# Kernel optimization log

Hardware: AMD Instinct MI355X
Metric: run time of the kernel (lower is better)

## Reference

```python
import jax, jax.numpy as jnp
import numpy as np

B, H, W, C = 1, 72, 72, 768
NH, HD = 12, 64
FF = 3072
EPS = 1e-6
THETA = 10000.0
S = H * W


def _rope_tables():
    freqs = 1.0 / THETA ** (np.arange(0, HD, 4, dtype=np.float32) / HD)  # [16]
    t = np.arange(H, dtype=np.float32)
    fx = np.outer(t, freqs)  # [72,16]
    fy = np.outer(t, freqs)
    fx = np.tile(fx[:, None, :], (1, W, 1))  # [72,72,16]
    fy = np.tile(fy[None, :, :], (H, 1, 1))
    fxy = np.concatenate([fx, fy], axis=-1).reshape(S, -1)  # [5184,32]
    fxy = np.repeat(fxy, 2, axis=-1)  # [5184,64]
    return jnp.asarray(np.cos(fxy)), jnp.asarray(np.sin(fxy))


def _rotate_pairwise(x):
    x1 = x[..., ::2]
    x2 = x[..., 1::2]
    return jnp.stack([-x2, x1], axis=-1).reshape(x.shape)


def _layernorm(x, g, b):
    m = jnp.mean(x, axis=-1, keepdims=True)
    v = jnp.mean(jnp.square(x - m), axis=-1, keepdims=True)
    return (x - m) * jax.lax.rsqrt(v + EPS) * g + b


def setup_inputs() -> dict:
    key = jax.random.key(0)
    ks = jax.random.split(key, 12)
    s_c = 1.0 / np.sqrt(C)
    s_ff = 1.0 / np.sqrt(FF)
    d = {
        "hidden_states": jax.random.normal(ks[0], (B, H, W, C), jnp.float32),
        "wq": jax.random.normal(ks[1], (C, C), jnp.float32) * s_c,
        "bq": jnp.zeros((C,), jnp.float32),
        "wk": jax.random.normal(ks[2], (C, C), jnp.float32) * s_c,
        "bk": jnp.zeros((C,), jnp.float32),
        "wv": jax.random.normal(ks[3], (C, C), jnp.float32) * s_c,
        "bv": jnp.zeros((C,), jnp.float32),
        "wo": jax.random.normal(ks[4], (C, C), jnp.float32) * s_c,
        "bo": jnp.zeros((C,), jnp.float32),
        "g1": jnp.ones((C,), jnp.float32),
        "b1": jnp.zeros((C,), jnp.float32),
        "g2": jnp.ones((C,), jnp.float32),
        "b2": jnp.zeros((C,), jnp.float32),
        "w_fc1": jax.random.normal(ks[5], (C, FF), jnp.float32) * s_c,
        "b_fc1": jnp.zeros((FF,), jnp.float32),
        "w_fc2": jax.random.normal(ks[6], (FF, C), jnp.float32) * s_ff,
        "b_fc2": jnp.zeros((C,), jnp.float32),
        "ls1": jnp.full((C,), 1e-5, jnp.float32),
        "ls2": jnp.full((C,), 1e-5, jnp.float32),
    }
    return d


def reference(hidden_states, wq, bq, wk, bk, wv, bv, wo, bo, g1, b1, g2, b2,
              w_fc1, b_fc1, w_fc2, b_fc2, ls1, ls2):
    cos, sin = _rope_tables()  # [S, HD]
    cos = cos[None, None]  # [1,1,S,HD]
    sin = sin[None, None]

    residual = hidden_states
    x = hidden_states.reshape(B, S, C)
    x = _layernorm(x, g1, b1)

    # attention
    q = (x @ wq + bq).reshape(B, S, NH, HD).transpose(0, 2, 1, 3)
    k = (x @ wk + bk).reshape(B, S, NH, HD).transpose(0, 2, 1, 3)
    v = (x @ wv + bv).reshape(B, S, NH, HD).transpose(0, 2, 1, 3)
    q = q * cos + _rotate_pairwise(q) * sin
    k = k * cos + _rotate_pairwise(k) * sin
    scale = HD ** -0.5
    attn = jax.nn.softmax(jnp.einsum('bhqd,bhkd->bhqk', q, k) * scale, axis=-1)
    o = jnp.einsum('bhqk,bhkd->bhqd', attn, v)
    o = o.transpose(0, 2, 1, 3).reshape(B, S, C)
    o = o @ wo + bo
    o = o * ls1

    hs = residual + o.reshape(B, H, W, C)
    residual = hs
    x = _layernorm(hs.reshape(B, S, C), g2, b2)
    x = jax.nn.gelu(x @ w_fc1 + b_fc1, approximate=False)
    x = x @ w_fc2 + b_fc2
    x = x * ls2
    return residual + x.reshape(B, H, W, C)
```

## Files before the change

### kernel.cpp

```cpp
#include <hip/hip_runtime.h>

#define S_  5184
#define C_  768
#define NH_ 12
#define HD_ 64
#define FF_ 3072
#define WW_ 72

typedef __attribute__((ext_vector_type(8))) short bf16x8;
typedef __attribute__((ext_vector_type(4))) float f32x4;

__device__ __forceinline__ float bf2f(unsigned short u){
    unsigned int i = ((unsigned int)u) << 16; float f; __builtin_memcpy(&f,&i,4); return f;
}
__device__ __forceinline__ unsigned short f2bf(float f){
    unsigned int i; __builtin_memcpy(&i,&f,4);
    unsigned int r = (i + 0x7fffu + ((i>>16)&1u)) >> 16;
    return (unsigned short)r;
}
__device__ __forceinline__ float ldf(float v){ return v; }
__device__ __forceinline__ float ldf(unsigned short v){ return bf2f(v); }

__device__ __forceinline__ void gload16(const void* g, const void* l) {
    __builtin_amdgcn_global_load_lds((const __attribute__((address_space(1))) void*)g,
                                     (__attribute__((address_space(3))) void*)l, 16, 0, 0);
}
__device__ __forceinline__ unsigned int cvtpk(float lo, float hi){
    unsigned int r;
    asm volatile("v_cvt_pk_bf16_f32 %0, %1, %2" : "=v"(r) : "v"(lo), "v"(hi));
    return r;
}

template<typename TIN>
__global__ __launch_bounds__(256) void ln_k(const TIN* __restrict__ x,
                                            const float* __restrict__ g,
                                            const float* __restrict__ b,
                                            unsigned short* __restrict__ out)
{
    int row = blockIdx.x, tid = threadIdx.x;
    const TIN* xr = x + (size_t)row * C_;
    float v0 = ldf(xr[tid]), v1 = ldf(xr[tid+256]), v2 = ldf(xr[tid+512]);
    float s = v0+v1+v2, q = v0*v0+v1*v1+v2*v2;
    #pragma unroll
    for (int off=32; off; off>>=1){ s += __shfl_xor(s,off); q += __shfl_xor(q,off); }
    __shared__ float ss[4], qq[4], mshare[2];
    int lane = tid & 63, wv = tid >> 6;
    if (!lane){ ss[wv] = s; qq[wv] = q; }
    __syncthreads();
    if (!tid){
        float S2 = ss[0]+ss[1]+ss[2]+ss[3];
        float Q2 = qq[0]+qq[1]+qq[2]+qq[3];
        float mean = S2 * (1.f/C_);
        float var  = Q2 * (1.f/C_) - mean*mean;
        mshare[0] = mean; mshare[1] = rsqrtf(var + 1e-6f);
    }
    __syncthreads();
    float mean = mshare[0], inv = mshare[1];
    unsigned short* orow = out + (size_t)row * C_;
    orow[tid]     = f2bf((v0-mean)*inv*g[tid]     + b[tid]);
    orow[tid+256] = f2bf((v1-mean)*inv*g[tid+256] + b[tid+256]);
    orow[tid+512] = f2bf((v2-mean)*inv*g[tid+512] + b[tid+512]);
}

__global__ __launch_bounds__(256) void rope_k(unsigned short* __restrict__ q,
                                              unsigned short* __restrict__ k)
{
    int idx = blockIdx.x * 256 + threadIdx.x;
    if (idx >= S_*32) return;
    int s = idx >> 5, i = idx & 31;
    int hh = s / WW_, ww = s % WW_;
    int m = i & 15;
    float coord = (i < 16) ? (float)hh : (float)ww;
    float freq = powf(10000.0f, -(float)m / 16.0f);
    float a = coord * freq;
    float c = cosf(a), sn = sinf(a);
    const float QS = 0.18033688011112042f;
    #pragma unroll
    for (int h = 0; h < NH_; h++) {
        size_t base = (size_t)s*C_ + h*HD_ + 2*i;
        float x0 = bf2f(q[base]), x1 = bf2f(q[base+1]);
        q[base]   = f2bf((x0*c - x1*sn) * QS);
        q[base+1] = f2bf((x1*c + x0*sn) * QS);
        x0 = bf2f(k[base]); x1 = bf2f(k[base+1]);
        k[base]   = f2bf(x0*c - x1*sn);
        k[base+1] = f2bf(x1*c + x0*sn);
    }
}

__global__ __launch_bounds__(256) void transpose_all(const float* __restrict__ wq, unsigned short* __restrict__ wqT,
                                                     const float* __restrict__ wk, unsigned short* __restrict__ wkT,
                                                     const float* __restrict__ wv, unsigned short* __restrict__ wvT,
                                                     const float* __restrict__ wo, unsigned short* __restrict__ woT,
                                                     const float* __restrict__ wf1, unsigned short* __restrict__ wf1T,
                                                     const float* __restrict__ wf2, unsigned short* __restrict__ wf2T)
{
    __shared__ float t[32][33];
    int b = blockIdx.x;
    const float* W; unsigned short* WT; int K, N, tb;
    if      (b < 576)  { W = wq;  WT = wqT;  K = 768;  N = 768;  tb = b; }
    else if (b < 1152) { W = wk;  WT = wkT;  K = 768;  N = 768;  tb = b - 576; }
    else if (b < 1728) { W = wv;  WT = wvT;  K = 768;  N = 768;  tb = b - 1152; }
    else if (b < 2304) { W = wo;  WT = woT;  K = 768;  N = 768;  tb = b - 1728; }
    else if (b < 4608) { W = wf1; WT = wf1T; K = 768;  N = 3072; tb = b - 2304; }
    else               { W = wf2; WT = wf2T; K = 3072; N = 768;  tb = b - 4608; }
    int ntx = N / 32;
    int n0 = (tb % ntx) * 32, k0 = (tb / ntx) * 32;
    int tx = threadIdx.x & 31, ty = threadIdx.x >> 5;
    #pragma unroll
    for (int i = 0; i < 4; i++)
        t[ty + i*8][tx] = W[(size_t)(k0 + ty + i*8)*N + n0 + tx];
    __syncthreads();
    #pragma unroll
    for (int i = 0; i < 4; i++)
        WT[(size_t)(n0 + ty + i*8)*K + k0 + tx] = f2bf(t[tx][ty + i*8]);
}

template<int EPI, int NWC, int BK>
__global__ __launch_bounds__(256) void gemm_mfma(const unsigned short* __restrict__ A,
                                                 const unsigned short* __restrict__ BT,
                                                 const float* __restrict__ bias,
                                                 const float* __restrict__ biasB,
                                                 const float* __restrict__ biasC,
                                                 const float* __restrict__ scale,
                                                 const float* __restrict__ addend,
                                                 void* __restrict__ outp,
                                                 void* __restrict__ outp2,
                                                 int M, int N, int K)
{
    const int BN = 64*NWC;
    const int MI = (NWC == 2) ? 4 : 2;
    __shared__ __align__(16) unsigned short As[2][128*BK];
    __shared__ __align__(16) unsigned short Bs[2][64*NWC*BK];
    int tid = threadIdx.x;
    int w = tid >> 6, lane = tid & 63, lq = lane & 15, lk = lane >> 4;
    int wr = (NWC == 2) ? (w >> 1) : w;
    int wc = (NWC == 2) ? (w & 1) : 0;

    int gx = gridDim.x;
    int nwg = gx * gridDim.y;
    int bid = blockIdx.y * gx + blockIdx.x;
    int xcd = bid & 7, idx = bid >> 3;
    int qq = nwg >> 3, rr = nwg & 7;
    int wg = (xcd < rr) ? (xcd*(qq+1) + idx) : (rr*(qq+1) + (xcd-rr)*qq + idx);
    int bm = (wg / gx) * 128, bn = (wg % gx) * BN;

    f32x4 acc[MI][4];
    #pragma unroll
    for (int i = 0; i < MI; i++)
        #pragma unroll
        for (int j = 0; j < 4; j++) acc[i][j] = 0;

    auto STAGE = [&](int buf, int kt) {
        #pragma unroll
        for (int u = 0; u < BK/16; u++) {
            int t = w*(BK/16) + u;
            int c = t*64 + lane;
            int kg = c >> 7, row = c & 127;
            int ra = bm + row; if (ra >= M) ra = M - 1;
            gload16(A + (size_t)ra*K + kt*BK + kg*8, As[buf] + t*512);
        }
        #pragma unroll
        for (int u = 0; u < BK*NWC/32; u++) {
            int t = w*(BK*NWC/32) + u;
            int c = t*64 + lane;
            int kg = (NWC == 2) ? (c >> 7) : (c >> 6);
            int row = (NWC == 2) ? (c & 127) : (c & 63);
            gload16(BT + (size_t)(bn + row)*K + kt*BK + kg*8, Bs[buf] + t*512);
        }
    };

    int nk = K / BK;
    STAGE(0, 0);
    int cur = 0;
    for (int kt = 0; kt < nk; kt++) {
        __syncthreads();
        if (kt + 1 < nk) STAGE(cur ^ 1, kt + 1);
        #pragma unroll
        for (int kk = 0; kk < BK/32; kk++) {
            bf16x8 af[MI], bfr[4];
            #pragma unroll
            for (int mi = 0; mi < MI; mi++)
                af[mi] = *(const bf16x8*)(As[cur] + (kk*4 + lk)*1024 + (wr*MI*16 + mi*16 + lq)*8);
            #pragma unroll
            for (int ni = 0; ni < 4; ni++)
                bfr[ni] = *(const bf16x8*)(Bs[cur] + (kk*4 + lk)*BN*8 + (wc*64 + ni*16 + lq)*8);
            #pragma unroll
            for (int mi = 0; mi < MI; mi++)
                #pragma unroll
                for (int ni = 0; ni < 4; ni++)
                    acc[mi][ni] = __builtin_amdgcn_mfma_f32_16x16x32_bf16(af[mi], bfr[ni], acc[mi][ni], 0, 0, 0);
        }
        cur ^= 1;
    }

    #pragma unroll
    for (int mi = 0; mi < MI; mi++) {
        #pragma unroll
        for (int ni = 0; ni < 4; ni++) {
            int n = bn + wc*64 + ni*16 + lq;
            int m0 = bm + wr*MI*16 + mi*16 + lk*4;
            if (EPI == 4) {
                if (n < 1536) {
                    const float* bb = (n < 768) ? bias : biasB;
                    int nn = (n < 768) ? n : (n - 768);
                    size_t base = (n < 768) ? 0 : ((size_t)S_ * 768);
                    #pragma unroll
                    for (int r = 0; r < 4; r++) {
                        int m = m0 + r;
                        if (m < M)
                            ((unsigned short*)outp)[base + (size_t)m*768 + nn] = f2bf(acc[mi][ni][r] + bb[nn]);
                    }
                } else {
                    if (m0 < M) {
                        float bv = biasC[n - 1536];
                        ushort4 pv;
                        pv.x = f2bf(acc[mi][ni][0] + bv);
                        pv.y = f2bf(acc[mi][ni][1] + bv);
                        pv.z = f2bf(acc[mi][ni][2] + bv);
                        pv.w = f2bf(acc[mi][ni][3] + bv);
                        *(ushort4*)((unsigned short*)outp2 + (size_t)(n - 1536)*S_ + m0) = pv;
                    }
                }
            } else {
                #pragma unroll
                for (int r = 0; r < 4; r++) {
                    int m = m0 + r;
                    if (m < M) {
                        float v = acc[mi][ni][r] + bias[n];
                        if (EPI == 1) {
                            v = 0.5f * v * (1.f + erff(v * 0.70710678f));
                            ((unsigned short*)outp)[(size_t)m*N + n] = f2bf(v);
                        } else {
                            size_t o = (size_t)m*N + n;
                            ((float*)outp)[o] = v*scale[n] + addend[o];
                        }
                    }
                }
            }
        }
    }
}

__global__ __launch_bounds__(256) void attn_mfma6(const unsigned short* __restrict__ Q,
                                                  const unsigned short* __restrict__ Kb,
                                                  const unsigned short* __restrict__ Vt,
                                                  unsigned short* __restrict__ O)
{
    __shared__ __align__(16) unsigned short Ks[2][4096];
    __shared__ __align__(16) unsigned short Vs[2][4096];
    int tid = threadIdx.x;
    int w = tid >> 6, lane = tid & 63, lq = lane & 15, lk = lane >> 4;
    int h = blockIdx.y;
    int q0 = blockIdx.x * 128 + w * 32;

    bf16x8 qf[2][2];
    #pragma unroll
    for (int qi = 0; qi < 2; qi++) {
        int qr = q0 + qi*16 + lq; if (qr >= S_) qr = S_ - 1;
        #pragma unroll
        for (int ks = 0; ks < 2; ks++)
            qf[qi][ks] = *(const bf16x8*)(Q + (size_t)qr*C_ + h*64 + ks*32 + lk*8);
    }

    union { bf16x8 v; unsigned int u[4]; } ones;
    ones.u[0] = 0x3F803F80u; ones.u[1] = 0x3F803F80u;
    ones.u[2] = 0x3F803F80u; ones.u[3] = 0x3F803F80u;

    f32x4 oacc[2][4];
    #pragma unroll
    for (int qi = 0; qi < 2; qi++)
        #pragma unroll
        for (int df = 0; df < 4; df++) oacc[qi][df] = 0;
    f32x4 lacc[2];
    lacc[0] = 0; lacc[1] = 0;

    auto STAGE = [&](int buf, int t) {
        int kv0 = t * 64;
        #pragma unroll
        for (int u = 0; u < 4; u++) {
            int tt = w*4 + u;
            if (tt < 8)
                gload16(Kb + (size_t)(kv0 + lane)*C_ + h*64 + tt*8, Ks[buf] + tt*512);
            else
                gload16(Vt + (size_t)(h*64 + lane)*S_ + kv0 + (tt-8)*8, Vs[buf] + (tt-8)*512);
        }
    };

    auto BODY = [&](int buf) {
        f32x4 s[2][4];
        #pragma unroll
        for (int qi = 0; qi < 2; qi++)
            #pragma unroll
            for (int nf = 0; nf < 4; nf++) s[qi][nf] = -8.0f;
        __builtin_amdgcn_s_setprio(1);
        #pragma unroll
        for (int ks = 0; ks < 2; ks++) {
            #pragma unroll
            for (int nf = 0; nf < 4; nf++) {
                bf16x8 kf = *(const bf16x8*)(Ks[buf] + (ks*4 + lk)*512 + (nf*16 + lq)*8);
                #pragma unroll
                for (int qi = 0; qi < 2; qi++)
                    s[qi][nf] = __builtin_amdgcn_mfma_f32_16x16x32_bf16(kf, qf[qi][ks], s[qi][nf], 0, 0, 0);
            }
        }
        __builtin_amdgcn_s_setprio(0);

        unsigned int pk[2][8];
        #pragma unroll
        for (int qi = 0; qi < 2; qi++) {
            #pragma unroll
            for (int nf = 0; nf < 4; nf++) {
                float p0 = exp2f(s[qi][nf][0]);
                float p1 = exp2f(s[qi][nf][1]);
                float p2 = exp2f(s[qi][nf][2]);
                float p3 = exp2f(s[qi][nf][3]);
                pk[qi][nf*2+0] = cvtpk(p0, p1);
                pk[qi][nf*2+1] = cvtpk(p2, p3);
            }
        }

        __builtin_amdgcn_s_setprio(1);
        #pragma unroll
        for (int ks = 0; ks < 2; ks++) {
            union { bf16x8 v; unsigned int u[4]; } pb[2];
            #pragma unroll
            for (int qi = 0; qi < 2; qi++) {
                pb[qi].u[0] = pk[qi][4*ks+0]; pb[qi].u[1] = pk[qi][4*ks+1];
                pb[qi].u[2] = pk[qi][4*ks+2]; pb[qi].u[3] = pk[qi][4*ks+3];
                lacc[qi] = __builtin_amdgcn_mfma_f32_16x16x32_bf16(ones.v, pb[qi].v, lacc[qi], 0, 0, 0);
            }
            #pragma unroll
            for (int df = 0; df < 4; df++) {
                int d = df*16 + lq;
                union { bf16x8 v; unsigned long long dd[2]; } va;
                va.dd[0] = *(const unsigned long long*)(Vs[buf] + (4*ks + (lk>>1))*512 + d*8 + (lk&1)*4);
                va.dd[1] = *(const unsigned long long*)(Vs[buf] + (4*ks + 2 + (lk>>1))*512 + d*8 + (lk&1)*4);
                #pragma unroll
                for (int qi = 0; qi < 2; qi++)
                    oacc[qi][df] = __builtin_amdgcn_mfma_f32_16x16x32_bf16(va.v, pb[qi].v, oacc[qi][df], 0, 0, 0);
            }
        }
        __builtin_amdgcn_s_setprio(0);
    };

    STAGE(0, 0);
    #pragma unroll 1
    for (int t = 0; t < 80; t += 2) {
        __syncthreads();
        STAGE(1, t + 1);
        BODY(0);
        __syncthreads();
        STAGE(0, t + 2);
        BODY(1);
    }
    __syncthreads();
    BODY(0);

    #pragma unroll
    for (int qi = 0; qi < 2; qi++) {
        int q = q0 + qi*16 + lq;
        if (q < S_) {
            float rl = 1.f / lacc[qi][0];
            #pragma unroll
            for (int df = 0; df < 4; df++) {
                ushort4 pv;
                pv.x = f2bf(oacc[qi][df][0] * rl);
                pv.y = f2bf(oacc[qi][df][1] * rl);
                pv.z = f2bf(oacc[qi][df][2] * rl);
                pv.w = f2bf(oacc[qi][df][3] * rl);
                *(ushort4*)(O + (size_t)q*C_ + h*64 + df*16 + lk*4) = pv;
            }
        }
    }
}

extern "C" void kernel_launch(void* const* d_in, const int* in_sizes, int n_in,
                              void* d_out, int out_size, void* d_ws, size_t ws_size,
                              hipStream_t stream)
{
    const float* hidden = (const float*)d_in[0];
    const float* wq  = (const float*)d_in[1];
    const float* bq  = (const float*)d_in[2];
    const float* wk  = (const float*)d_in[3];
    const float* bk  = (const float*)d_in[4];
    const float* wv  = (const float*)d_in[5];
    const float* bv  = (const float*)d_in[6];
    const float* wo  = (const float*)d_in[7];
    const float* bo  = (const float*)d_in[8];
    const float* g1  = (const float*)d_in[9];
    const float* b1  = (const float*)d_in[10];
    const float* g2  = (const float*)d_in[11];
    const float* b2  = (const float*)d_in[12];
    const float* wf1 = (const float*)d_in[13];
    const float* bf1 = (const float*)d_in[14];
    const float* wf2 = (const float*)d_in[15];
    const float* bf2_ = (const float*)d_in[16];
    const float* ls1 = (const float*)d_in[17];
    const float* ls2 = (const float*)d_in[18];

    char* ws = (char*)d_ws;
    size_t off = 0;
    auto alloc = [&](size_t bytes) { char* p = ws + off; off += (bytes + 255) & ~(size_t)255; return p; };

    float* res1          = (float*)alloc((size_t)S_*C_*4);
    unsigned short* lnb  = (unsigned short*)alloc((size_t)S_*C_*2);
    unsigned short* qb   = (unsigned short*)alloc((size_t)S_*C_*2);
    unsigned short* kb   = (unsigned short*)alloc((size_t)S_*C_*2);
    unsigned short* vtb  = (unsigned short*)alloc((size_t)S_*C_*2);
    unsigned short* ob   = (unsigned short*)alloc((size_t)S_*C_*2);
    unsigned short* fc1b = qb;
    unsigned short* wqT  = (unsigned short*)alloc((size_t)C_*C_*2);
    unsigned short* wkT  = (unsigned short*)alloc((size_t)C_*C_*2);
    unsigned short* wvT  = (unsigned short*)alloc((size_t)C_*C_*2);
    unsigned short* woT  = (unsigned short*)alloc((size_t)C_*C_*2);
    unsigned short* wf1T = (unsigned short*)alloc((size_t)C_*FF_*2);
    unsigned short* wf2T = (unsigned short*)alloc((size_t)C_*FF_*2);
    float* outb = (float*)d_out;

    hipLaunchKernelGGL(transpose_all, dim3(6912), dim3(256), 0, stream,
                       wq, wqT, wk, wkT, wv, wvT, wo, woT, wf1, wf1T, wf2, wf2T);
    hipLaunchKernelGGL(ln_k<float>, dim3(S_), dim3(256), 0, stream, hidden, g1, b1, lnb);
    hipLaunchKernelGGL((gemm_mfma<4,2,32>), dim3(2304/128, 41), dim3(256), 0, stream,
                       lnb, wqT, bq, bk, bv, (const float*)nullptr, (const float*)nullptr,
                       (void*)qb, (void*)vtb, S_, 2304, C_);
    hipLaunchKernelGGL(rope_k, dim3((S_*32 + 255)/256), dim3(256), 0, stream, qb, kb);
    hipLaunchKernelGGL(attn_mfma6, dim3((S_ + 127)/128, NH_), dim3(256), 0, stream,
                       qb, kb, vtb, ob);
    hipLaunchKernelGGL((gemm_mfma<2,1,64>), dim3(C_/64, 41), dim3(256), 0, stream,
                       ob, woT, bo, (const float*)nullptr, (const float*)nullptr, ls1, hidden,
                       (void*)res1, (void*)nullptr, S_, C_, C_);
    hipLaunchKernelGGL(ln_k<float>, dim3(S_), dim3(256), 0, stream, res1, g2, b2, lnb);
    hipLaunchKernelGGL((gemm_mfma<1,2,32>), dim3(FF_/128, 41), dim3(256), 0, stream,
                       lnb, wf1T, bf1, (const float*)nullptr, (const float*)nullptr,
                       (const float*)nullptr, (const float*)nullptr,
                       (void*)fc1b, (void*)nullptr, S_, FF_, C_);
    hipLaunchKernelGGL((gemm_mfma<2,1,64>), dim3(C_/64, 41), dim3(256), 0, stream,
                       fc1b, wf2T, bf2_, (const float*)nullptr, (const float*)nullptr, ls2, res1,
                       (void*)outb, (void*)nullptr, S_, C_, FF_);
    (void)in_sizes; (void)n_in; (void)out_size; (void)ws_size;
}
```

Baseline: 426.2 us.

## Split-K by two for output-projection and FC2 GEMMs with combine kernel

Adds a split-K epilogue mode that writes bf16 partial products for each K half, indexed by blockIdx.z, and a separate combine kernel that sums the partials and applies bias, layer scale and the residual. The O-projection and FC2 GEMMs, which have only 768 output columns, now launch twice as many workgroups to fill the GPU better and shorten each block's K loop. In exchange it adds an extra partial-buffer round trip through memory, an extra kernel launch per GEMM, and rounding of the partial sums to bf16.

```diff
diff --git a/kernel.cpp b/kernel.cpp
--- a/kernel.cpp
+++ b/kernel.cpp
@@ -125,7 +125,7 @@
                                                  const float* __restrict__ addend,
                                                  void* __restrict__ outp,
                                                  void* __restrict__ outp2,
-                                                 int M, int N, int K)
+                                                 int M, int N, int K, int lda)
 {
     const int BN = 64*NWC;
     const int MI = (NWC == 2) ? 4 : 2;
@@ -136,6 +136,11 @@
     int wr = (NWC == 2) ? (w >> 1) : w;
     int wc = (NWC == 2) ? (w & 1) : 0;
 
+    if (EPI == 5) {
+        A  += (size_t)blockIdx.z * K;
+        BT += (size_t)blockIdx.z * K;
+    }
+
     int gx = gridDim.x;
     int nwg = gx * gridDim.y;
     int bid = blockIdx.y * gx + blockIdx.x;
@@ -157,7 +162,7 @@
             int c = t*64 + lane;
             int kg = c >> 7, row = c & 127;
             int ra = bm + row; if (ra >= M) ra = M - 1;
-            gload16(A + (size_t)ra*K + kt*BK + kg*8, As[buf] + t*512);
+            gload16(A + (size_t)ra*lda + kt*BK + kg*8, As[buf] + t*512);
         }
         #pragma unroll
         for (int u = 0; u < BK*NWC/32; u++) {
@@ -165,7 +170,7 @@
             int c = t*64 + lane;
             int kg = (NWC == 2) ? (c >> 7) : (c >> 6);
             int row = (NWC == 2) ? (c & 127) : (c & 63);
-            gload16(BT + (size_t)(bn + row)*K + kt*BK + kg*8, Bs[buf] + t*512);
+            gload16(BT + (size_t)(bn + row)*lda + kt*BK + kg*8, Bs[buf] + t*512);
         }
     };
 
@@ -221,6 +226,13 @@
                         *(ushort4*)((unsigned short*)outp2 + (size_t)(n - 1536)*S_ + m0) = pv;
                     }
                 }
+            } else if (EPI == 5) {
+                unsigned short* pp = (unsigned short*)outp + (size_t)blockIdx.z * ((size_t)M * N);
+                #pragma unroll
+                for (int r = 0; r < 4; r++) {
+                    int m = m0 + r;
+                    if (m < M) pp[(size_t)m*N + n] = f2bf(acc[mi][ni][r]);
+                }
             } else {
                 #pragma unroll
                 for (int r = 0; r < 4; r++) {
@@ -239,6 +251,26 @@
             }
         }
     }
+}
+
+__global__ __launch_bounds__(256) void comb_k(const unsigned short* __restrict__ p,
+                                              const float* __restrict__ bias,
+                                              const float* __restrict__ scale,
+                                              const float* __restrict__ addend,
+                                              float* __restrict__ out)
+{
+    int gid = blockIdx.x * 256 + threadIdx.x;
+    if (gid >= S_*C_/4) return;
+    int n = (gid % (C_/4)) * 4;
+    ushort4 a = ((const ushort4*)p)[gid];
+    ushort4 b = ((const ushort4*)(p + (size_t)S_*C_))[gid];
+    float4 ad = ((const float4*)addend)[gid];
+    float4 o;
+    o.x = (bf2f(a.x) + bf2f(b.x) + bias[n+0]) * scale[n+0] + ad.x;
+    o.y = (bf2f(a.y) + bf2f(b.y) + bias[n+1]) * scale[n+1] + ad.y;
+    o.z = (bf2f(a.z) + bf2f(b.z) + bias[n+2]) * scale[n+2] + ad.z;
+    o.w = (bf2f(a.w) + bf2f(b.w) + bias[n+3]) * scale[n+3] + ad.w;
+    ((float4*)out)[gid] = o;
 }
 
 __global__ __launch_bounds__(256) void attn_mfma6(const unsigned short* __restrict__ Q,
@@ -415,6 +447,7 @@
     unsigned short* woT  = (unsigned short*)alloc((size_t)C_*C_*2);
     unsigned short* wf1T = (unsigned short*)alloc((size_t)C_*FF_*2);
     unsigned short* wf2T = (unsigned short*)alloc((size_t)C_*FF_*2);
+    unsigned short* pbuf = (unsigned short*)alloc((size_t)2*S_*C_*2);
     float* outb = (float*)d_out;
 
     hipLaunchKernelGGL(transpose_all, dim3(6912), dim3(256), 0, stream,
@@ -422,20 +455,26 @@
     hipLaunchKernelGGL(ln_k<float>, dim3(S_), dim3(256), 0, stream, hidden, g1, b1, lnb);
     hipLaunchKernelGGL((gemm_mfma<4,2,32>), dim3(2304/128, 41), dim3(256), 0, stream,
                        lnb, wqT, bq, bk, bv, (const float*)nullptr, (const float*)nullptr,
-                       (void*)qb, (void*)vtb, S_, 2304, C_);
+                       (void*)qb, (void*)vtb, S_, 2304, C_, C_);
     hipLaunchKernelGGL(rope_k, dim3((S_*32 + 255)/256), dim3(256), 0, stream, qb, kb);
     hipLaunchKernelGGL(attn_mfma6, dim3((S_ + 127)/128, NH_), dim3(256), 0, stream,
                        qb, kb, vtb, ob);
-    hipLaunchKernelGGL((gemm_mfma<2,1,64>), dim3(C_/64, 41), dim3(256), 0, stream,
-                       ob, woT, bo, (const float*)nullptr, (const float*)nullptr, ls1, hidden,
-                       (void*)res1, (void*)nullptr, S_, C_, C_);
+    hipLaunchKernelGGL((gemm_mfma<5,1,64>), dim3(C_/64, 41, 2), dim3(256), 0, stream,
+                       ob, woT, (const float*)nullptr, (const float*)nullptr, (const float*)nullptr,
+                       (const float*)nullptr, (const float*)nullptr,
+                       (void*)pbuf, (void*)nullptr, S_, C_, C_/2, C_);
+    hipLaunchKernelGGL(comb_k, dim3((S_*C_/4 + 255)/256), dim3(256), 0, stream,
+                       pbuf, bo, ls1, hidden, res1);
     hipLaunchKernelGGL(ln_k<float>, dim3(S_), dim3(256), 0, stream, res1, g2, b2, lnb);
     hipLaunchKernelGGL((gemm_mfma<1,2,32>), dim3(FF_/128, 41), dim3(256), 0, stream,
                        lnb, wf1T, bf1, (const float*)nullptr, (const float*)nullptr,
                        (const float*)nullptr, (const float*)nullptr,
-                       (void*)fc1b, (void*)nullptr, S_, FF_, C_);
-    hipLaunchKernelGGL((gemm_mfma<2,1,64>), dim3(C_/64, 41), dim3(256), 0, stream,
-                       fc1b, wf2T, bf2_, (const float*)nullptr, (const float*)nullptr, ls2, res1,
-                       (void*)outb, (void*)nullptr, S_, C_, FF_);
+                       (void*)fc1b, (void*)nullptr, S_, FF_, C_, C_);
+    hipLaunchKernelGGL((gemm_mfma<5,1,64>), dim3(C_/64, 41, 2), dim3(256), 0, stream,
+                       fc1b, wf2T, (const float*)nullptr, (const float*)nullptr, (const float*)nullptr,
+                       (const float*)nullptr, (const float*)nullptr,
+                       (void*)pbuf, (void*)nullptr, S_, C_, FF_/2, FF_);
+    hipLaunchKernelGGL(comb_k, dim3((S_*C_/4 + 255)/256), dim3(256), 0, stream,
+                       pbuf, bf2_, ls2, res1, outb);
     (void)in_sizes; (void)n_in; (void)out_size; (void)ws_size;
 }
```

After: 443.6 us. +4.1%, slower.
